# Optimization experiments

Measured on AMD Instinct MI355X. Metric: run time of the kernel, lower is better.

The kernel has to match this reference:

```python
import jax, jax.numpy as jnp
import numpy as np

N_X_POINTS = 100
IN_FEATURES = 2
OUT_FEATURES = 512
BATCH = 8192


def make_grid():
    # torch.meshgrid default indexing='ij'; stack flattened, transpose -> [K, in_features]
    axes = [jnp.linspace(0.0, 1.0, N_X_POINTS, dtype=jnp.float32) for _ in range(IN_FEATURES)]
    mesh = jnp.meshgrid(*axes, indexing='ij')
    return jnp.stack([m.ravel() for m in mesh]).T  # [10000, 2]


def setup_inputs() -> dict:
    key = jax.random.key(0)
    k1, k2, k3, k4 = jax.random.split(key, 4)
    X = jax.random.normal(k1, (BATCH, OUT_FEATURES), dtype=jnp.float32)
    # nn.Linear(in_features=2, out_features=512): weight [512, 2], bias [512]
    W = jax.random.normal(k2, (OUT_FEATURES, IN_FEATURES), dtype=jnp.float32) * (1.0 / np.sqrt(IN_FEATURES))
    b = jax.random.normal(k3, (OUT_FEATURES,), dtype=jnp.float32) * 0.1
    betta = jax.random.uniform(k4, (1,), dtype=jnp.float32)  # torch.rand(1)
    grid = make_grid()
    return {"X": X, "W": W, "b": b, "betta": betta, "grid": grid}


def reference(X, W, b, betta, grid):
    # GTMEstimator.transform with method='mean', mean=0, std=1.
    yg = grid @ W.T + b                                   # y(grid): [K, D]
    # squared euclidean distances: cdist(yg, X)^2 -> [K, N]
    d2 = (jnp.sum(yg * yg, axis=1)[:, None]
          + jnp.sum(X * X, axis=1)[None, :]
          - 2.0 * (yg @ X.T))
    logits = (-betta[0] / 2.0) * d2                       # [K, N]
    # p = (betta/2pi)^(D/2) * exp(logits); p_x = p / p.sum(axis=0).
    # The constant cancels in normalization, so this is exactly softmax over the grid axis
    # (numerically stable form of the original computation).
    p_x = jax.nn.softmax(logits, axis=0)                  # [K, N]
    return p_x.T @ grid                                   # (grid.T @ p_x).T -> [N, in_features]
```

## Files before the change

### kernel.cpp

```cpp
#include <hip/hip_runtime.h>
#include <math.h>

#ifndef __has_builtin
#define __has_builtin(x) 0
#endif
#if __has_builtin(__builtin_amdgcn_exp2f)
#define EXP2F(x) __builtin_amdgcn_exp2f(x)
#else
#define EXP2F(x) exp2f(x)
#endif

typedef float v2f __attribute__((ext_vector_type(2)));

namespace {

constexpr int DIM    = 512;
constexpr int NBATCH = 8192;
constexpr int WPB    = 4;
constexpr int SPW    = 2;
constexpr int BLOCK  = WPB * 64;
constexpr float INV99 = 1.0f / 99.0f;
constexpr float LOG2E = 1.4426950408889634f;

__global__ __launch_bounds__(BLOCK) void gtm_final_kernel(
    const float* __restrict__ X, const float* __restrict__ W,
    const float* __restrict__ b, const float* __restrict__ betta,
    float* __restrict__ out) {
  __shared__ float sER[WPB][100][SPW];
  __shared__ float sEC[WPB][128][SPW];

  const int lane = threadIdx.x & 63;
  const int wave = threadIdx.x >> 6;
  const int n0 = blockIdx.x * (WPB * SPW) + wave * SPW;

  float4 xr[SPW][2];
  #pragma unroll
  for (int s = 0; s < SPW; ++s) {
    const float4* Xv = reinterpret_cast<const float4*>(X + (size_t)(n0 + s) * DIM);
    xr[s][0] = Xv[lane * 2];
    xr[s][1] = Xv[lane * 2 + 1];
  }
  float w0[8], w1[8], bb[8];
  {
    const float4* Wv = reinterpret_cast<const float4*>(W);
    #pragma unroll
    for (int j = 0; j < 4; ++j) {
      float4 wv = Wv[lane * 4 + j];
      w0[2*j]   = wv.x; w1[2*j]   = wv.y;
      w0[2*j+1] = wv.z; w1[2*j+1] = wv.w;
    }
    const float4* bv = reinterpret_cast<const float4*>(b);
    float4 ba = bv[lane*2], bc = bv[lane*2+1];
    bb[0]=ba.x; bb[1]=ba.y; bb[2]=ba.z; bb[3]=ba.w;
    bb[4]=bc.x; bb[5]=bc.y; bb[6]=bc.z; bb[7]=bc.w;
  }

  float q11=0.f, q12=0.f, q22=0.f, u0=0.f, u1=0.f;
  #pragma unroll
  for (int j = 0; j < 8; ++j) {
    q11 = fmaf(w0[j], w0[j], q11); q12 = fmaf(w0[j], w1[j], q12);
    q22 = fmaf(w1[j], w1[j], q22);
    u0  = fmaf(w0[j], bb[j], u0);  u1  = fmaf(w1[j], bb[j], u1);
  }
  float pa[SPW], pc[SPW];
  #pragma unroll
  for (int s = 0; s < SPW; ++s) {
    float xx[8] = {xr[s][0].x, xr[s][0].y, xr[s][0].z, xr[s][0].w,
                   xr[s][1].x, xr[s][1].y, xr[s][1].z, xr[s][1].w};
    float a = 0.f, c = 0.f;
    #pragma unroll
    for (int j = 0; j < 8; ++j) {
      a = fmaf(w0[j], xx[j], a);
      c = fmaf(w1[j], xx[j], c);
    }
    pa[s] = a; pc[s] = c;
  }
  #pragma unroll
  for (int off = 32; off; off >>= 1) {
    q11 += __shfl_xor(q11, off, 64); q12 += __shfl_xor(q12, off, 64);
    q22 += __shfl_xor(q22, off, 64);
    u0  += __shfl_xor(u0,  off, 64); u1  += __shfl_xor(u1,  off, 64);
    #pragma unroll
    for (int s = 0; s < SPW; ++s) {
      pa[s] += __shfl_xor(pa[s], off, 64);
      pc[s] += __shfl_xor(pc[s], off, 64);
    }
  }

  const float lam = betta[0] * LOG2E;
  const float cX  = -lam * q12;
  const float aF  = -0.5f * lam * q11, aG = -0.5f * lam * q22;
  const float gi1 = lane * INV99, gi2 = (lane + 64) * INV99;
  const bool hiOk = (lane + 64) < 100;

  const float gaF1 = aF * gi1 * gi1, gaF2 = aF * gi2 * gi2;
  const float gaG1 = aG * gi1 * gi1, gaG2 = aG * gi2 * gi2;

  float f1[SPW], f2[SPW], h1[SPW], h2[SPW], mF[SPW], mG[SPW];
  #pragma unroll
  for (int s = 0; s < SPW; ++s) {
    const float bF = lam * (pa[s] - u0), bG = lam * (pc[s] - u1);
    f1[s] = fmaf(gi1, bF, gaF1);
    f2[s] = fmaf(gi2, bF, gaF2);
    h1[s] = fmaf(gi1, bG, gaG1);
    h2[s] = fmaf(gi2, bG, gaG2);
    mF[s] = fmaxf(f1[s], hiOk ? f2[s] : -3.0e38f);
    mG[s] = fmaxf(h1[s], hiOk ? h2[s] : -3.0e38f);
  }
  #pragma unroll
  for (int off = 32; off; off >>= 1) {
    #pragma unroll
    for (int s = 0; s < SPW; ++s) {
      mF[s] = fmaxf(mF[s], __shfl_xor(mF[s], off, 64));
      mG[s] = fmaxf(mG[s], __shfl_xor(mG[s], off, 64));
    }
  }

  #pragma unroll
  for (int s = 0; s < SPW; ++s) {
    sER[wave][lane][s] = EXP2F(f1[s] - mF[s]);
    sEC[wave][lane][s] = EXP2F(h1[s] - mG[s]);
    if (hiOk) {
      sER[wave][lane + 64][s] = EXP2F(f2[s] - mF[s]);
      sEC[wave][lane + 64][s] = EXP2F(h2[s] - mG[s]);
    } else {
      sEC[wave][lane + 64][s] = 0.f;
    }
  }
  __syncthreads();

  const float r1 = EXP2F(cX * gi1 * INV99);
  const float r2 = EXP2F(cX * gi2 * INV99);
  float pw1 = 1.f, pw2 = 1.f, g0r = 0.f;

  v2f T1 = (v2f)0.f, T2 = (v2f)0.f, U1 = (v2f)0.f, U2 = (v2f)0.f;

  for (int c = 0; c < 25; ++c) {
    const float4 ea = *reinterpret_cast<const float4*>(&sER[wave][4*c][0]);
    const float4 eb = *reinterpret_cast<const float4*>(&sER[wave][4*c + 2][0]);
    const v2f er_[4] = {{ea.x, ea.y}, {ea.z, ea.w}, {eb.x, eb.y}, {eb.z, eb.w}};
    #pragma unroll
    for (int j = 0; j < 4; ++j) {
      const v2f er = er_[j];
      T1 += er * pw1;
      T2 += er * pw2;
      const v2f erg = er * g0r;
      U1 += erg * pw1;
      U2 += erg * pw2;
      pw1 *= r1; pw2 *= r2; g0r += INV99;
    }
  }

  v2f ec1v = {sEC[wave][lane][0],      sEC[wave][lane][1]};
  v2f ec2v = {sEC[wave][lane + 64][0], sEC[wave][lane + 64][1]};
  v2f ct1 = ec1v * T1, ct2 = ec2v * T2;
  v2f S   = ct1 + ct2;
  v2f Sg0 = ec1v * U1 + ec2v * U2;
  v2f Sg1 = ct1 * gi1 + ct2 * gi2;

  #pragma unroll
  for (int off = 32; off; off >>= 1) {
    S.x   += __shfl_xor(S.x,   off, 64); S.y   += __shfl_xor(S.y,   off, 64);
    Sg0.x += __shfl_xor(Sg0.x, off, 64); Sg0.y += __shfl_xor(Sg0.y, off, 64);
    Sg1.x += __shfl_xor(Sg1.x, off, 64); Sg1.y += __shfl_xor(Sg1.y, off, 64);
  }
  if (lane < SPW) {
    const float sv = lane ? S.y   : S.x;
    const float g0 = lane ? Sg0.y : Sg0.x;
    const float g1 = lane ? Sg1.y : Sg1.x;
    const float inv = 1.f / sv;
    reinterpret_cast<float2*>(out)[n0 + lane] = make_float2(g0 * inv, g1 * inv);
  }
}

}

extern "C" void kernel_launch(void* const* d_in, const int* in_sizes, int n_in,
                              void* d_out, int out_size, void* d_ws, size_t ws_size,
                              hipStream_t stream) {
  const float* X     = (const float*)d_in[0];
  const float* W     = (const float*)d_in[1];
  const float* b     = (const float*)d_in[2];
  const float* betta = (const float*)d_in[3];
  float* out = (float*)d_out;
  (void)d_ws; (void)ws_size;

  gtm_final_kernel<<<NBATCH / (WPB * SPW), BLOCK, 0, stream>>>(X, W, b, betta, out);
}
```

Before: 15.71 us.

## Compute softmax max analytically, precompute weighted table, split power-chain accumulators

Replaces the wave-wide max shuffle reduction with a closed-form maximum of the concave quadratic, found by clamping its vertex to [0,1]. The shared table now stores both exp values and grid-weighted exp values as float4, which removes the per-step g0r multiply. The inner loop keeps four independent accumulator sets, advanced by r^4 per step and recombined at the end, to shorten dependency chains. It also drops the __syncthreads, which is safe only because each wave reads just its own shared slice. The trade-offs are more registers, and the continuous vertex maximum can exceed the true maximum over grid points, which shifts the exponent offset slightly.

```diff
diff --git a/kernel.cpp b/kernel.cpp
--- a/kernel.cpp
+++ b/kernel.cpp
@@ -26,7 +26,7 @@
     const float* __restrict__ X, const float* __restrict__ W,
     const float* __restrict__ b, const float* __restrict__ betta,
     float* __restrict__ out) {
-  __shared__ float sER[WPB][100][SPW];
+  __shared__ float sTab[WPB][100][4];
   __shared__ float sEC[WPB][128][SPW];
 
   const int lane = threadIdx.x & 63;
@@ -93,69 +93,82 @@
   const float gi1 = lane * INV99, gi2 = (lane + 64) * INV99;
   const bool hiOk = (lane + 64) < 100;
 
+  const float rcpF = -1.f / (2.f * aF);
+  const float rcpG = -1.f / (2.f * aG);
+  float mF[SPW], mG[SPW], bFv[SPW], bGv[SPW];
+  #pragma unroll
+  for (int s = 0; s < SPW; ++s) {
+    const float bF = lam * (pa[s] - u0), bG = lam * (pc[s] - u1);
+    bFv[s] = bF; bGv[s] = bG;
+    float gf = fminf(fmaxf(bF * rcpF, 0.f), 1.f);
+    float gg = fminf(fmaxf(bG * rcpG, 0.f), 1.f);
+    mF[s] = gf * fmaf(aF, gf, bF);
+    mG[s] = gg * fmaf(aG, gg, bG);
+  }
+
   const float gaF1 = aF * gi1 * gi1, gaF2 = aF * gi2 * gi2;
   const float gaG1 = aG * gi1 * gi1, gaG2 = aG * gi2 * gi2;
-
-  float f1[SPW], f2[SPW], h1[SPW], h2[SPW], mF[SPW], mG[SPW];
-  #pragma unroll
-  for (int s = 0; s < SPW; ++s) {
-    const float bF = lam * (pa[s] - u0), bG = lam * (pc[s] - u1);
-    f1[s] = fmaf(gi1, bF, gaF1);
-    f2[s] = fmaf(gi2, bF, gaF2);
-    h1[s] = fmaf(gi1, bG, gaG1);
-    h2[s] = fmaf(gi2, bG, gaG2);
-    mF[s] = fmaxf(f1[s], hiOk ? f2[s] : -3.0e38f);
-    mG[s] = fmaxf(h1[s], hiOk ? h2[s] : -3.0e38f);
-  }
-  #pragma unroll
-  for (int off = 32; off; off >>= 1) {
-    #pragma unroll
-    for (int s = 0; s < SPW; ++s) {
-      mF[s] = fmaxf(mF[s], __shfl_xor(mF[s], off, 64));
-      mG[s] = fmaxf(mG[s], __shfl_xor(mG[s], off, 64));
-    }
-  }
-
-  #pragma unroll
-  for (int s = 0; s < SPW; ++s) {
-    sER[wave][lane][s] = EXP2F(f1[s] - mF[s]);
-    sEC[wave][lane][s] = EXP2F(h1[s] - mG[s]);
+  {
+    float er0 = EXP2F(fmaf(gi1, bFv[0], gaF1) - mF[0]);
+    float er1 = EXP2F(fmaf(gi1, bFv[1], gaF1) - mF[1]);
+    *reinterpret_cast<float4*>(&sTab[wave][lane][0]) =
+        make_float4(er0, er1, gi1 * er0, gi1 * er1);
+    sEC[wave][lane][0] = EXP2F(fmaf(gi1, bGv[0], gaG1) - mG[0]);
+    sEC[wave][lane][1] = EXP2F(fmaf(gi1, bGv[1], gaG1) - mG[1]);
     if (hiOk) {
-      sER[wave][lane + 64][s] = EXP2F(f2[s] - mF[s]);
-      sEC[wave][lane + 64][s] = EXP2F(h2[s] - mG[s]);
+      float e20 = EXP2F(fmaf(gi2, bFv[0], gaF2) - mF[0]);
+      float e21 = EXP2F(fmaf(gi2, bFv[1], gaF2) - mF[1]);
+      *reinterpret_cast<float4*>(&sTab[wave][lane + 64][0]) =
+          make_float4(e20, e21, gi2 * e20, gi2 * e21);
+      sEC[wave][lane + 64][0] = EXP2F(fmaf(gi2, bGv[0], gaG2) - mG[0]);
+      sEC[wave][lane + 64][1] = EXP2F(fmaf(gi2, bGv[1], gaG2) - mG[1]);
     } else {
-      sEC[wave][lane + 64][s] = 0.f;
-    }
-  }
-  __syncthreads();
+      sEC[wave][lane + 64][0] = 0.f;
+      sEC[wave][lane + 64][1] = 0.f;
+    }
+  }
 
   const float r1 = EXP2F(cX * gi1 * INV99);
   const float r2 = EXP2F(cX * gi2 * INV99);
-  float pw1 = 1.f, pw2 = 1.f, g0r = 0.f;
-
-  v2f T1 = (v2f)0.f, T2 = (v2f)0.f, U1 = (v2f)0.f, U2 = (v2f)0.f;
-
+  float R1 = r1 * r1; R1 *= R1;
+  float R2 = r2 * r2; R2 *= R2;
+  float pw1 = 1.f, pw2 = 1.f;
+
+  v2f T1[4], U1[4], T2[4], U2[4];
+  #pragma unroll
+  for (int m = 0; m < 4; ++m) {
+    T1[m]=(v2f)0.f; U1[m]=(v2f)0.f; T2[m]=(v2f)0.f; U2[m]=(v2f)0.f;
+  }
+
+  const float4* tab = reinterpret_cast<const float4*>(&sTab[wave][0][0]);
   for (int c = 0; c < 25; ++c) {
-    const float4 ea = *reinterpret_cast<const float4*>(&sER[wave][4*c][0]);
-    const float4 eb = *reinterpret_cast<const float4*>(&sER[wave][4*c + 2][0]);
-    const v2f er_[4] = {{ea.x, ea.y}, {ea.z, ea.w}, {eb.x, eb.y}, {eb.z, eb.w}};
-    #pragma unroll
-    for (int j = 0; j < 4; ++j) {
-      const v2f er = er_[j];
-      T1 += er * pw1;
-      T2 += er * pw2;
-      const v2f erg = er * g0r;
-      U1 += erg * pw1;
-      U2 += erg * pw2;
-      pw1 *= r1; pw2 *= r2; g0r += INV99;
-    }
-  }
-
-  v2f ec1v = {sEC[wave][lane][0],      sEC[wave][lane][1]};
-  v2f ec2v = {sEC[wave][lane + 64][0], sEC[wave][lane + 64][1]};
-  v2f ct1 = ec1v * T1, ct2 = ec2v * T2;
+    float4 t[4];
+    t[0] = tab[4*c];     t[1] = tab[4*c + 1];
+    t[2] = tab[4*c + 2]; t[3] = tab[4*c + 3];
+    #pragma unroll
+    for (int m = 0; m < 4; ++m) {
+      const v2f er  = {t[m].x, t[m].y};
+      const v2f erg = {t[m].z, t[m].w};
+      T1[m] += er  * pw1;
+      U1[m] += erg * pw1;
+      T2[m] += er  * pw2;
+      U2[m] += erg * pw2;
+    }
+    pw1 *= R1; pw2 *= R2;
+  }
+
+  const float r1b = r1 * r1, r1c = r1b * r1;
+  const float r2b = r2 * r2, r2c = r2b * r2;
+  v2f Tc1 = T1[0] + r1*T1[1] + r1b*T1[2] + r1c*T1[3];
+  v2f Uc1 = U1[0] + r1*U1[1] + r1b*U1[2] + r1c*U1[3];
+  v2f Tc2 = T2[0] + r2*T2[1] + r2b*T2[2] + r2c*T2[3];
+  v2f Uc2 = U2[0] + r2*U2[1] + r2b*U2[2] + r2c*U2[3];
+
+  const v2f ec1v = {sEC[wave][lane][0],      sEC[wave][lane][1]};
+  const v2f ec2v = {sEC[wave][lane + 64][0], sEC[wave][lane + 64][1]};
+  const v2f ct1 = ec1v * Tc1, ct2 = ec2v * Tc2;
   v2f S   = ct1 + ct2;
-  v2f Sg0 = ec1v * U1 + ec2v * U2;
+  v2f Sg0 = ec1v * Uc1 + ec2v * Uc2;
   v2f Sg1 = ct1 * gi1 + ct2 * gi2;
 
   #pragma unroll
```

After: 14.85 us, median of 2. 1.06x faster.
